# Performance work log

Measured on AMD Instinct MI355X. Metric: run time of the kernel, lower is better.

Reference implementation:

```python
import jax, jax.numpy as jnp
import numpy as np

D_MODEL = 1024
NHEAD = 16
HEAD_DIM = D_MODEL // NHEAD
WINDOW = 64


def setup_inputs() -> dict:
    key = jax.random.key(0)
    ks = jax.random.split(key, 5)
    B, S = 1, 4096
    x = jax.random.normal(ks[0], (B, S, D_MODEL), dtype=jnp.float32)
    scale = 0.02
    Wq = jax.random.normal(ks[1], (D_MODEL, D_MODEL), dtype=jnp.float32) * scale
    Wk = jax.random.normal(ks[2], (D_MODEL, D_MODEL), dtype=jnp.float32) * scale
    Wv = jax.random.normal(ks[3], (D_MODEL, D_MODEL), dtype=jnp.float32) * scale
    Wo = jax.random.normal(ks[4], (D_MODEL, D_MODEL), dtype=jnp.float32) * scale
    return {"x": x, "Wq": Wq, "Wk": Wk, "Wv": Wv, "Wo": Wo}


def reference(x, Wq, Wk, Wv, Wo):
    B, S, D = x.shape
    H, hd, W = NHEAD, HEAD_DIM, WINDOW
    # projections (torch Linear: y = x @ W.T)
    q = (x @ Wq.T).reshape(B, S, H, hd).transpose(0, 2, 1, 3)  # [B,H,S,hd]
    k = (x @ Wk.T).reshape(B, S, H, hd).transpose(0, 2, 1, 3)
    v = (x @ Wv.T).reshape(B, S, H, hd).transpose(0, 2, 1, 3)
    # sliding window indices: each query attends to [i-W+1, i]
    qpos = jnp.arange(S)
    offsets = jnp.arange(-W + 1, 1)
    key_idx = qpos[:, None] + offsets[None, :]          # [S,W]
    valid = (key_idx >= 0) & (key_idx < S)
    key_idx = jnp.clip(key_idx, 0, S - 1)
    # gather windows: [B,H,S,W,hd]
    kw = jnp.take(k, key_idx, axis=2)
    vw = jnp.take(v, key_idx, axis=2)
    scores = jnp.einsum('bhsd,bhswd->bhsw', q, kw) / (hd ** 0.5)
    scores = jnp.where(valid[None, None, :, :], scores, -jnp.inf)
    attn = jax.nn.softmax(scores, axis=-1)
    out = jnp.einsum('bhsw,bhswd->bhsd', attn, vw)      # [B,H,S,hd]
    out = out.transpose(0, 2, 1, 3).reshape(B, S, D)
    return out @ Wo.T
```

## Files before the change

### kernel.cpp

```cpp
#include <hip/hip_runtime.h>
#include <cstdint>

typedef unsigned short u16;
using bf16x8 = __attribute__((ext_vector_type(8))) short;
using u16x8  = __attribute__((ext_vector_type(8))) unsigned short;
using f32x4  = __attribute__((ext_vector_type(4))) float;

#define DM 1024

__device__ __forceinline__ u16 f2b(float f) {
    union { float f; unsigned u; } v; v.f = f;
    unsigned r = v.u + 0x7FFFu + ((v.u >> 16) & 1u);
    return (u16)(r >> 16);
}

#define GLL(gp, lp) __builtin_amdgcn_global_load_lds( \
    (const __attribute__((address_space(1))) void*)(uintptr_t)(gp), \
    (__attribute__((address_space(3))) void*)(unsigned)(uintptr_t)(lp), 16, 0, 0)

#define BAR()    __builtin_amdgcn_s_barrier()
#define WAITV6() asm volatile("s_waitcnt vmcnt(6)" ::: "memory")
#define WAITV5() asm volatile("s_waitcnt vmcnt(5)" ::: "memory")
#define WAITV0() asm volatile("s_waitcnt vmcnt(0)" ::: "memory")

__global__ __launch_bounds__(256) void cvt_all(const float* __restrict__ x,
                                               const float* __restrict__ Wq,
                                               const float* __restrict__ Wk,
                                               const float* __restrict__ Wv,
                                               const float* __restrict__ Wo,
                                               u16* __restrict__ xb,
                                               u16* __restrict__ wqkv,
                                               u16* __restrict__ wob) {
    size_t v = ((size_t)blockIdx.x * 256 + threadIdx.x) << 3;
    const float* src; u16* dst; size_t off; float sc = 1.0f;
    if (v < (size_t)4194304) { src = x; dst = xb; off = v; }
    else {
        size_t w = v - 4194304; int s = (int)(w >> 20); off = w & 1048575;
        src = (s == 0) ? Wq : (s == 1) ? Wk : (s == 2) ? Wv : Wo;
        dst = (s < 3) ? (wqkv + ((size_t)s << 20)) : wob;
        if (s == 0) sc = 0.125f;
    }
    const f32x4* p = (const f32x4*)(src + off);
    f32x4 a = p[0], b = p[1];
    u16x8 o;
    o[0] = f2b(a[0] * sc); o[1] = f2b(a[1] * sc); o[2] = f2b(a[2] * sc); o[3] = f2b(a[3] * sc);
    o[4] = f2b(b[0] * sc); o[5] = f2b(b[1] * sc); o[6] = f2b(b[2] * sc); o[7] = f2b(b[3] * sc);
    *(u16x8*)(dst + off) = o;
}

#define MROW3(af_, bf_, d) \
    acc[d][0] = __builtin_amdgcn_mfma_f32_16x16x32_bf16(af_, bf_[0], acc[d][0], 0, 0, 0); \
    acc[d][1] = __builtin_amdgcn_mfma_f32_16x16x32_bf16(af_, bf_[1], acc[d][1], 0, 0, 0); \
    acc[d][2] = __builtin_amdgcn_mfma_f32_16x16x32_bf16(af_, bf_[2], acc[d][2], 0, 0, 0);

#define MFMA12(af_, bf_) do { \
    __builtin_amdgcn_s_setprio(1); \
    MROW3(af_[0], bf_, 0) \
    MROW3(af_[1], bf_, 1) \
    MROW3(af_[2], bf_, 2) \
    MROW3(af_[3], bf_, 3) \
    __builtin_amdgcn_s_setprio(0); } while (0)

__global__ __launch_bounds__(512, 4) void gemm_qkv8(const u16* __restrict__ A,
                                                    const u16* __restrict__ B,
                                                    u16* __restrict__ QKV) {
    __shared__ __align__(16) u16 As[2 * 8192];
    __shared__ __align__(16) u16 Bs[2 * 12288];
    const int tid  = threadIdx.x;
    const int lane = tid & 63;
    const int wid  = tid >> 6;
    const int wr   = wid >> 2;
    const int wc   = wid & 3;
    const int fr   = lane & 15;
    const int fg   = lane >> 4;

    const int hw  = blockIdx.y * 16 + blockIdx.x;
    const int xcd = hw & 7;
    const int idx = hw >> 3;
    const int reg = xcd + ((idx >> 4) << 3);
    const int mt  = ((reg >> 2) << 2) + ((idx & 15) >> 2);
    const int nt  = ((reg & 3) << 2) + (idx & 3);
    const int brow = mt << 7;
    const int bcol = nt * 192;

    const int srow = tid >> 3;
    const int scol = ((tid & 7) ^ (srow & 7)) << 3;
    const u16* Ag = A + (size_t)(brow + srow) * 1024 + scol;
    const u16* Bg = B + (size_t)(bcol + srow) * 1024 + scol;

#define STG_A(buf, kt, c) GLL(Ag + (size_t)(c) * 65536 + (kt) * 64, \
                              (char*)As + (buf) * 16384 + (c) * 8192 + (wid << 10))
#define STG_B(buf, kt, c) GLL(Bg + (size_t)(c) * 65536 + (kt) * 64, \
                              (char*)Bs + (buf) * 24576 + (c) * 8192 + (wid << 10))
#define STG(buf, kt) do { \
        STG_A(buf, kt, 0); STG_A(buf, kt, 1); \
        STG_B(buf, kt, 0); STG_B(buf, kt, 1); STG_B(buf, kt, 2); } while (0)

    const int swz  = (fr & 7) << 3;
    const int col0 = (fg << 3) ^ swz;
    const int col1 = (32 + (fg << 3)) ^ swz;
    const int aro  = ((wr << 6) + fr) << 6;
    const int bro  = ((wc * 48) + fr) << 6;

#define LDA4(dst, bufo, cl) do { \
    const u16* p_ = As + (bufo) + aro + (cl); \
    dst[0] = *(const bf16x8*)(p_); \
    dst[1] = *(const bf16x8*)(p_ + 1024); \
    dst[2] = *(const bf16x8*)(p_ + 2048); \
    dst[3] = *(const bf16x8*)(p_ + 3072); } while (0)

#define LDB3(dst, bufo, cl) do { \
    const u16* p_ = Bs + (bufo) + bro + (cl); \
    dst[0] = *(const bf16x8*)(p_); \
    dst[1] = *(const bf16x8*)(p_ + 1024); \
    dst[2] = *(const bf16x8*)(p_ + 2048); } while (0)

    f32x4 acc[4][3];
    const f32x4 z = {0.f, 0.f, 0.f, 0.f};
    #pragma unroll
    for (int i = 0; i < 4; ++i)
        #pragma unroll
        for (int j = 0; j < 3; ++j) acc[i][j] = z;

    bf16x8 af0[4], af1[4], bf0[3], bf1[3];

    STG(0, 0);
    STG(1, 1);

    #pragma unroll 1
    for (int t = 0; t < 14; ++t) {
        const int bo  = (t & 1) ? 8192 : 0;
        const int bob = (t & 1) ? 12288 : 0;
        WAITV5();
        BAR();
        LDA4(af0, bo, col0); LDB3(bf0, bob, col0);
        MFMA12(af0, bf0);
        LDA4(af1, bo, col1); LDB3(bf1, bob, col1);
        MFMA12(af1, bf1);
        BAR();
        STG(t & 1, t + 2);
    }
    WAITV5(); BAR();
    LDA4(af0, 0, col0); LDB3(bf0, 0, col0);
    MFMA12(af0, bf0);
    LDA4(af1, 0, col1); LDB3(bf1, 0, col1);
    MFMA12(af1, bf1);
    WAITV0(); BAR();
    LDA4(af0, 8192, col0); LDB3(bf0, 12288, col0);
    MFMA12(af0, bf0);
    LDA4(af1, 8192, col1); LDB3(bf1, 12288, col1);
    MFMA12(af1, bf1);

    const int ocol0 = bcol + wc * 48;
    const int orow0 = brow + (wr << 6);
    #pragma unroll
    for (int i = 0; i < 4; ++i)
        #pragma unroll
        for (int j = 0; j < 3; ++j)
            #pragma unroll
            for (int r = 0; r < 4; ++r) {
                const int row = orow0 + i * 16 + fg * 4 + r;
                const int col = ocol0 + j * 16 + fr;
                QKV[(size_t)row * 3072 + col] = f2b(acc[i][j][r]);
            }
#undef STG_A
#undef STG_B
#undef STG
#undef LDA4
#undef LDB3
}

__global__ __launch_bounds__(256) void gemm_out(const u16* __restrict__ A,
                                                const u16* __restrict__ B,
                                                float* __restrict__ C) {
    __shared__ __align__(16) u16 As[2 * 8192];
    __shared__ __align__(16) u16 Bs[2 * 4096];
    const int tid  = threadIdx.x;
    const int lane = tid & 63;
    const int wid  = tid >> 6;
    const int wr   = wid >> 1;
    const int wc   = wid & 1;
    const int fr   = lane & 15;
    const int fg   = lane >> 4;

    const int hw  = blockIdx.y * 16 + blockIdx.x;
    const int xcd = hw & 7;
    const int idx = hw >> 3;
    const int reg = xcd + ((idx >> 4) << 3);
    const int mt  = ((reg >> 2) << 2) + ((idx & 15) >> 2);
    const int nt  = ((reg & 3) << 2) + (idx & 3);
    const int brow = mt << 7;
    const int bcol = nt << 6;

    const int srow = tid >> 3;
    const int scol = ((tid & 7) ^ (srow & 7)) << 3;
    const u16* Ag = A + (size_t)(brow + srow) * 1024 + scol;
    const u16* Bg = B + (size_t)(bcol + srow) * 1024 + scol;

#define OSTG_A(buf, kt, c) GLL(Ag + (size_t)(c) * 32768 + (kt) * 64, \
                               (char*)As + (buf) * 16384 + (c) * 4096 + (tid << 4))
#define OSTG_B(buf, kt, c) GLL(Bg + (size_t)(c) * 32768 + (kt) * 64, \
                               (char*)Bs + (buf) * 8192 + (c) * 4096 + (tid << 4))
#define OSTG(buf, kt) do { \
        OSTG_A(buf, kt, 0); OSTG_A(buf, kt, 1); OSTG_A(buf, kt, 2); OSTG_A(buf, kt, 3); \
        OSTG_B(buf, kt, 0); OSTG_B(buf, kt, 1); } while (0)

    const int swz  = (fr & 7) << 3;
    const int col0 = (fg << 3) ^ swz;
    const int col1 = (32 + (fg << 3)) ^ swz;
    const int aro  = ((wr << 6) + fr) << 6;
    const int bro  = ((wc << 5) + fr) << 6;

    f32x4 acc[4][2];
    const f32x4 z = {0.f, 0.f, 0.f, 0.f};
    #pragma unroll
    for (int i = 0; i < 4; ++i) { acc[i][0] = z; acc[i][1] = z; }

#define OCOMP(bufo4, bufo3) do { \
        const u16* Ab = As + (bufo4); \
        const u16* Bb = Bs + (bufo3); \
        bf16x8 a0[4], a1[4], b0[2], b1[2]; \
        _Pragma("unroll") \
        for (int i = 0; i < 4; ++i) { \
            a0[i] = *(const bf16x8*)(Ab + aro + (i << 10) + col0); \
            a1[i] = *(const bf16x8*)(Ab + aro + (i << 10) + col1); \
        } \
        _Pragma("unroll") \
        for (int j = 0; j < 2; ++j) { \
            b0[j] = *(const bf16x8*)(Bb + bro + (j << 10) + col0); \
            b1[j] = *(const bf16x8*)(Bb + bro + (j << 10) + col1); \
        } \
        __builtin_amdgcn_s_setprio(1); \
        _Pragma("unroll") \
        for (int i = 0; i < 4; ++i) \
            _Pragma("unroll") \
            for (int j = 0; j < 2; ++j) { \
                acc[i][j] = __builtin_amdgcn_mfma_f32_16x16x32_bf16(a0[i], b0[j], acc[i][j], 0, 0, 0); \
                acc[i][j] = __builtin_amdgcn_mfma_f32_16x16x32_bf16(a1[i], b1[j], acc[i][j], 0, 0, 0); \
            } \
        __builtin_amdgcn_s_setprio(0); } while (0)

    OSTG(0, 0);
    OSTG(1, 1);

    #pragma unroll 1
    for (int t = 0; t < 14; ++t) {
        const int bo4 = (t & 1) ? 8192 : 0;
        const int bo3 = (t & 1) ? 4096 : 0;
        WAITV6();
        BAR();
        OCOMP(bo4, bo3);
        BAR();
        OSTG(t & 1, t + 2);
    }
    WAITV6(); BAR();
    OCOMP(0, 0);
    WAITV0(); BAR();
    OCOMP(8192, 4096);
#undef OSTG_A
#undef OSTG_B
#undef OSTG
#undef OCOMP

    #pragma unroll
    for (int i = 0; i < 4; ++i)
        #pragma unroll
        for (int j = 0; j < 2; ++j)
            #pragma unroll
            for (int r = 0; r < 4; ++r) {
                const int row = brow + wr * 64 + i * 16 + fg * 4 + r;
                const int col = bcol + wc * 32 + j * 16 + fr;
                C[(size_t)row * 1024 + col] = acc[i][j][r];
            }
}

__global__ __launch_bounds__(256) void attn_kernel(const u16* __restrict__ QKV,
                                                   u16* __restrict__ Og) {
    const int qb  = blockIdx.x;
    const int h   = blockIdx.y;
    const int tid = threadIdx.x;
    const int lane = tid & 63;
    const int w  = tid >> 6;
    const int fr = lane & 15;
    const int fg = lane >> 4;

    __shared__ __align__(16) u16 QK[64 * 72 + 128 * 72];
    __shared__ __align__(16) u16 Vt[64 * 138];
    __shared__ float Mrow[64][4];
    __shared__ float Lrow[64][4];

    u16* Qs = QK;
    u16* Ks = QK + 64 * 72;
    u16* Ps = QK;

    const u16* Qg = QKV;
    const u16* Kg = QKV + 1024;
    const u16* Vg = QKV + 2048;

    const int hoff  = h * 64;
    const int qrow0 = qb * 64;
    const int krow0 = qrow0 - 64;

    {
        const int r  = tid >> 3;
        const int c0 = (tid & 7) * 8;
        #pragma unroll
        for (int it = 0; it < 2; ++it) {
            const int row = r + it * 32;
            u16x8 val = *(const u16x8*)(Qg + (size_t)(qrow0 + row) * 3072 + hoff + c0);
            *(u16x8*)(Qs + row * 72 + c0) = val;
        }
        #pragma unroll
        for (int it = 0; it < 4; ++it) {
            const int row  = r + it * 32;
            const int grow = krow0 + row;
            u16x8 val = {0, 0, 0, 0, 0, 0, 0, 0};
            if (grow >= 0) val = *(const u16x8*)(Kg + (size_t)grow * 3072 + hoff + c0);
            *(u16x8*)(Ks + row * 72 + c0) = val;
        }
        #pragma unroll
        for (int it = 0; it < 4; ++it) {
            const int j    = r + it * 32;
            const int grow = krow0 + j;
            u16x8 val = {0, 0, 0, 0, 0, 0, 0, 0};
            if (grow >= 0) val = *(const u16x8*)(Vg + (size_t)grow * 3072 + hoff + c0);
            #pragma unroll
            for (int e = 0; e < 8; ++e) Vt[(c0 + e) * 138 + j] = val[e];
        }
    }
    __syncthreads();

    const f32x4 z = {0.f, 0.f, 0.f, 0.f};
    f32x4 s[4][2];
    #pragma unroll
    for (int i = 0; i < 4; ++i) { s[i][0] = z; s[i][1] = z; }
    #pragma unroll
    for (int kk = 0; kk < 2; ++kk) {
        const int k0 = kk * 32 + fg * 8;
        bf16x8 aq[4];
        #pragma unroll
        for (int i = 0; i < 4; ++i)
            aq[i] = *(const bf16x8*)(Qs + (i * 16 + fr) * 72 + k0);
        #pragma unroll
        for (int n = 0; n < 2; ++n) {
            const bf16x8 bk = *(const bf16x8*)(Ks + (w * 32 + n * 16 + fr) * 72 + k0);
            #pragma unroll
            for (int i = 0; i < 4; ++i)
                s[i][n] = __builtin_amdgcn_mfma_f32_16x16x32_bf16(aq[i], bk, s[i][n], 0, 0, 0);
        }
    }

    #pragma unroll
    for (int i = 0; i < 4; ++i) {
        #pragma unroll
        for (int r = 0; r < 4; ++r) {
            const int irow = i * 16 + fg * 4 + r;
            float mx = -3.0e38f;
            #pragma unroll
            for (int n = 0; n < 2; ++n) {
                const int jcol = w * 32 + n * 16 + fr;
                const bool valid = (jcol >= irow + 1) && (jcol <= irow + 64) && (krow0 + jcol >= 0);
                const float v = valid ? s[i][n][r] : -3.0e38f;
                s[i][n][r] = v;
                mx = fmaxf(mx, v);
            }
            #pragma unroll
            for (int d = 1; d < 16; d <<= 1) mx = fmaxf(mx, __shfl_xor(mx, d));
            if (fr == 0) Mrow[irow][w] = mx;
        }
    }
    __syncthreads();

    #pragma unroll
    for (int i = 0; i < 4; ++i) {
        #pragma unroll
        for (int r = 0; r < 4; ++r) {
            const int irow = i * 16 + fg * 4 + r;
            const float M = fmaxf(fmaxf(Mrow[irow][0], Mrow[irow][1]),
                                  fmaxf(Mrow[irow][2], Mrow[irow][3]));
            float sum = 0.f;
            #pragma unroll
            for (int n = 0; n < 2; ++n) {
                const float v = s[i][n][r];
                const float p = (v > -1.0e38f) ? __expf(v - M) : 0.f;
                sum += p;
                Ps[irow * 136 + (w * 32 + n * 16 + fr)] = f2b(p);
            }
            #pragma unroll
            for (int d = 1; d < 16; d <<= 1) sum += __shfl_xor(sum, d);
            if (fr == 0) Lrow[irow][w] = sum;
        }
    }
    __syncthreads();

    f32x4 o[4] = {z, z, z, z};
    #pragma unroll
    for (int ks = 0; ks < 4; ++ks) {
        const int k0 = ks * 32 + fg * 8;
        const bf16x8 ap = *(const bf16x8*)(Ps + (w * 16 + fr) * 136 + k0);
        #pragma unroll
        for (int n = 0; n < 4; ++n) {
            const bf16x8 bv = *(const bf16x8*)(Vt + (n * 16 + fr) * 138 + k0);
            o[n] = __builtin_amdgcn_mfma_f32_16x16x32_bf16(ap, bv, o[n], 0, 0, 0);
        }
    }

    #pragma unroll
    for (int r = 0; r < 4; ++r) {
        const int irow = w * 16 + fg * 4 + r;
        const float L = Lrow[irow][0] + Lrow[irow][1] + Lrow[irow][2] + Lrow[irow][3];
        const float rl = 1.0f / L;
        #pragma unroll
        for (int n = 0; n < 4; ++n)
            Og[(size_t)(qrow0 + irow) * DM + hoff + n * 16 + fr] = f2b(o[n][r] * rl);
    }
}

extern "C" void kernel_launch(void* const* d_in, const int* in_sizes, int n_in,
                              void* d_out, int out_size, void* d_ws, size_t ws_size,
                              hipStream_t stream) {
    (void)in_sizes; (void)n_in; (void)out_size; (void)ws_size;
    const float* x  = (const float*)d_in[0];
    const float* Wq = (const float*)d_in[1];
    const float* Wk = (const float*)d_in[2];
    const float* Wv = (const float*)d_in[3];
    const float* Wo = (const float*)d_in[4];
    float* out = (float*)d_out;

    char* ws = (char*)d_ws;
    u16* xb   = (u16*)(ws);
    u16* Wqkv = (u16*)(ws + ((size_t)8  << 20));
    u16* Wob  = (u16*)(ws + ((size_t)14 << 20));
    u16* qkvb = (u16*)(ws + ((size_t)16 << 20));
    u16* ab   = (u16*)(ws + ((size_t)40 << 20));

    cvt_all<<<4096, 256, 0, stream>>>(x, Wq, Wk, Wv, Wo, xb, Wqkv, Wob);
    gemm_qkv8<<<dim3(16, 32), 512, 0, stream>>>(xb, Wqkv, qkvb);
    attn_kernel<<<dim3(64, 16), 256, 0, stream>>>(qkvb, ab);
    gemm_out<<<dim3(16, 32), 256, 0, stream>>>(ab, Wob, out);
}
```

Baseline: 79.75 us.

## Fuse fp32-to-bf16 conversion into GEMM staging and drop separate convert kernel

Removes the standalone conversion kernel and has both GEMMs load fp32 x/weights directly, convert to bf16 in registers (applying the Q scale), and write swizzled tiles into LDS via register prefetch. The aim is to save a kernel launch and the extra write/read of bf16 copies in global memory. The trade-off is that GEMM staging moves from async global-to-LDS loads to register-based loads with conversion ALU work. It also reads twice as many bytes per tile, and the QKV GEMM's occupancy hint drops from 4 to 2 waves per SIMD. x is re-read and re-converted by each of the 16 column tiles.

```diff
diff --git a/kernel.cpp b/kernel.cpp
--- a/kernel.cpp
+++ b/kernel.cpp
@@ -14,39 +14,21 @@
     return (u16)(r >> 16);
 }
 
+__device__ __forceinline__ u16x8 cvt8(f32x4 a, f32x4 b, float sc) {
+    u16x8 o;
+    o[0] = f2b(a[0] * sc); o[1] = f2b(a[1] * sc);
+    o[2] = f2b(a[2] * sc); o[3] = f2b(a[3] * sc);
+    o[4] = f2b(b[0] * sc); o[5] = f2b(b[1] * sc);
+    o[6] = f2b(b[2] * sc); o[7] = f2b(b[3] * sc);
+    return o;
+}
+
 #define GLL(gp, lp) __builtin_amdgcn_global_load_lds( \
     (const __attribute__((address_space(1))) void*)(uintptr_t)(gp), \
     (__attribute__((address_space(3))) void*)(unsigned)(uintptr_t)(lp), 16, 0, 0)
 
 #define BAR()    __builtin_amdgcn_s_barrier()
-#define WAITV6() asm volatile("s_waitcnt vmcnt(6)" ::: "memory")
-#define WAITV5() asm volatile("s_waitcnt vmcnt(5)" ::: "memory")
 #define WAITV0() asm volatile("s_waitcnt vmcnt(0)" ::: "memory")
-
-__global__ __launch_bounds__(256) void cvt_all(const float* __restrict__ x,
-                                               const float* __restrict__ Wq,
-                                               const float* __restrict__ Wk,
-                                               const float* __restrict__ Wv,
-                                               const float* __restrict__ Wo,
-                                               u16* __restrict__ xb,
-                                               u16* __restrict__ wqkv,
-                                               u16* __restrict__ wob) {
-    size_t v = ((size_t)blockIdx.x * 256 + threadIdx.x) << 3;
-    const float* src; u16* dst; size_t off; float sc = 1.0f;
-    if (v < (size_t)4194304) { src = x; dst = xb; off = v; }
-    else {
-        size_t w = v - 4194304; int s = (int)(w >> 20); off = w & 1048575;
-        src = (s == 0) ? Wq : (s == 1) ? Wk : (s == 2) ? Wv : Wo;
-        dst = (s < 3) ? (wqkv + ((size_t)s << 20)) : wob;
-        if (s == 0) sc = 0.125f;
-    }
-    const f32x4* p = (const f32x4*)(src + off);
-    f32x4 a = p[0], b = p[1];
-    u16x8 o;
-    o[0] = f2b(a[0] * sc); o[1] = f2b(a[1] * sc); o[2] = f2b(a[2] * sc); o[3] = f2b(a[3] * sc);
-    o[4] = f2b(b[0] * sc); o[5] = f2b(b[1] * sc); o[6] = f2b(b[2] * sc); o[7] = f2b(b[3] * sc);
-    *(u16x8*)(dst + off) = o;
-}
 
 #define MROW3(af_, bf_, d) \
     acc[d][0] = __builtin_amdgcn_mfma_f32_16x16x32_bf16(af_, bf_[0], acc[d][0], 0, 0, 0); \
@@ -61,8 +43,10 @@
     MROW3(af_[3], bf_, 3) \
     __builtin_amdgcn_s_setprio(0); } while (0)
 
-__global__ __launch_bounds__(512, 4) void gemm_qkv8(const u16* __restrict__ A,
-                                                    const u16* __restrict__ B,
+__global__ __launch_bounds__(512, 2) void gemm_qkv8(const float* __restrict__ x,
+                                                    const float* __restrict__ Wq,
+                                                    const float* __restrict__ Wk,
+                                                    const float* __restrict__ Wv,
                                                     u16* __restrict__ QKV) {
     __shared__ __align__(16) u16 As[2 * 8192];
     __shared__ __align__(16) u16 Bs[2 * 12288];
@@ -84,17 +68,49 @@
     const int bcol = nt * 192;
 
     const int srow = tid >> 3;
-    const int scol = ((tid & 7) ^ (srow & 7)) << 3;
-    const u16* Ag = A + (size_t)(brow + srow) * 1024 + scol;
-    const u16* Bg = B + (size_t)(bcol + srow) * 1024 + scol;
-
-#define STG_A(buf, kt, c) GLL(Ag + (size_t)(c) * 65536 + (kt) * 64, \
-                              (char*)As + (buf) * 16384 + (c) * 8192 + (wid << 10))
-#define STG_B(buf, kt, c) GLL(Bg + (size_t)(c) * 65536 + (kt) * 64, \
-                              (char*)Bs + (buf) * 24576 + (c) * 8192 + (wid << 10))
-#define STG(buf, kt) do { \
-        STG_A(buf, kt, 0); STG_A(buf, kt, 1); \
-        STG_B(buf, kt, 0); STG_B(buf, kt, 1); STG_B(buf, kt, 2); } while (0)
+    const int cg   = tid & 7;
+    const int aD   = srow * 64 + ((cg ^ (srow & 7)) << 3);
+
+    const float* aSrc0 = x + (size_t)(brow + srow) * 1024 + cg * 8;
+    const float* aSrc1 = x + (size_t)(brow + 64 + srow) * 1024 + cg * 8;
+    const float* bSrc0; const float* bSrc1; const float* bSrc2;
+    float bScl0, bScl1, bScl2;
+    {
+        int g0 = bcol + srow, g1 = bcol + 64 + srow, g2 = bcol + 128 + srow;
+        bSrc0 = ((g0 < 1024) ? (Wq + (size_t)g0 * 1024)
+                 : (g0 < 2048) ? (Wk + (size_t)(g0 - 1024) * 1024)
+                               : (Wv + (size_t)(g0 - 2048) * 1024)) + cg * 8;
+        bScl0 = (g0 < 1024) ? 0.125f : 1.0f;
+        bSrc1 = ((g1 < 1024) ? (Wq + (size_t)g1 * 1024)
+                 : (g1 < 2048) ? (Wk + (size_t)(g1 - 1024) * 1024)
+                               : (Wv + (size_t)(g1 - 2048) * 1024)) + cg * 8;
+        bScl1 = (g1 < 1024) ? 0.125f : 1.0f;
+        bSrc2 = ((g2 < 1024) ? (Wq + (size_t)g2 * 1024)
+                 : (g2 < 2048) ? (Wk + (size_t)(g2 - 1024) * 1024)
+                               : (Wv + (size_t)(g2 - 2048) * 1024)) + cg * 8;
+        bScl2 = (g2 < 1024) ? 0.125f : 1.0f;
+    }
+
+    f32x4 la00, la01, la10, la11;
+    f32x4 lb00, lb01, lb10, lb11, lb20, lb21;
+
+#define ISSUE(kt) do { \
+    la00 = *(const f32x4*)(aSrc0 + (kt) * 64); la01 = *(const f32x4*)(aSrc0 + (kt) * 64 + 4); \
+    la10 = *(const f32x4*)(aSrc1 + (kt) * 64); la11 = *(const f32x4*)(aSrc1 + (kt) * 64 + 4); \
+    lb00 = *(const f32x4*)(bSrc0 + (kt) * 64); lb01 = *(const f32x4*)(bSrc0 + (kt) * 64 + 4); \
+    lb10 = *(const f32x4*)(bSrc1 + (kt) * 64); lb11 = *(const f32x4*)(bSrc1 + (kt) * 64 + 4); \
+    lb20 = *(const f32x4*)(bSrc2 + (kt) * 64); lb21 = *(const f32x4*)(bSrc2 + (kt) * 64 + 4); \
+} while (0)
+
+#define WRITE(bi) do { \
+    u16* Ad = As + (bi) * 8192 + aD; \
+    u16* Bd = Bs + (bi) * 12288 + aD; \
+    *(u16x8*)(Ad)        = cvt8(la00, la01, 1.0f); \
+    *(u16x8*)(Ad + 4096) = cvt8(la10, la11, 1.0f); \
+    *(u16x8*)(Bd)        = cvt8(lb00, lb01, bScl0); \
+    *(u16x8*)(Bd + 4096) = cvt8(lb10, lb11, bScl1); \
+    *(u16x8*)(Bd + 8192) = cvt8(lb20, lb21, bScl2); \
+} while (0)
 
     const int swz  = (fr & 7) << 3;
     const int col0 = (fg << 3) ^ swz;
@@ -124,28 +140,24 @@
 
     bf16x8 af0[4], af1[4], bf0[3], bf1[3];
 
-    STG(0, 0);
-    STG(1, 1);
+    ISSUE(0);
+    WRITE(0);
+    ISSUE(1);
 
     #pragma unroll 1
-    for (int t = 0; t < 14; ++t) {
+    for (int t = 0; t < 15; ++t) {
         const int bo  = (t & 1) ? 8192 : 0;
         const int bob = (t & 1) ? 12288 : 0;
-        WAITV5();
         BAR();
         LDA4(af0, bo, col0); LDB3(bf0, bob, col0);
         MFMA12(af0, bf0);
         LDA4(af1, bo, col1); LDB3(bf1, bob, col1);
         MFMA12(af1, bf1);
         BAR();
-        STG(t & 1, t + 2);
-    }
-    WAITV5(); BAR();
-    LDA4(af0, 0, col0); LDB3(bf0, 0, col0);
-    MFMA12(af0, bf0);
-    LDA4(af1, 0, col1); LDB3(bf1, 0, col1);
-    MFMA12(af1, bf1);
-    WAITV0(); BAR();
+        WRITE((t + 1) & 1);
+        if (t < 14) ISSUE(t + 2);
+    }
+    BAR();
     LDA4(af0, 8192, col0); LDB3(bf0, 12288, col0);
     MFMA12(af0, bf0);
     LDA4(af1, 8192, col1); LDB3(bf1, 12288, col1);
@@ -163,15 +175,14 @@
                 const int col = ocol0 + j * 16 + fr;
                 QKV[(size_t)row * 3072 + col] = f2b(acc[i][j][r]);
             }
-#undef STG_A
-#undef STG_B
-#undef STG
+#undef ISSUE
+#undef WRITE
 #undef LDA4
 #undef LDB3
 }
 
 __global__ __launch_bounds__(256) void gemm_out(const u16* __restrict__ A,
-                                                const u16* __restrict__ B,
+                                                const float* __restrict__ Wo,
                                                 float* __restrict__ C) {
     __shared__ __align__(16) u16 As[2 * 8192];
     __shared__ __align__(16) u16 Bs[2 * 4096];
@@ -193,17 +204,24 @@
     const int bcol = nt << 6;
 
     const int srow = tid >> 3;
-    const int scol = ((tid & 7) ^ (srow & 7)) << 3;
+    const int cg   = tid & 7;
+    const int scol = ((cg ^ (srow & 7)) << 3);
     const u16* Ag = A + (size_t)(brow + srow) * 1024 + scol;
-    const u16* Bg = B + (size_t)(bcol + srow) * 1024 + scol;
+    const float* bSrc0 = Wo + (size_t)(bcol + srow) * 1024 + cg * 8;
+    const float* bSrc1 = Wo + (size_t)(bcol + 32 + srow) * 1024 + cg * 8;
+    const int bD = srow * 64 + ((cg ^ (srow & 7)) << 3);
 
 #define OSTG_A(buf, kt, c) GLL(Ag + (size_t)(c) * 32768 + (kt) * 64, \
                                (char*)As + (buf) * 16384 + (c) * 4096 + (tid << 4))
-#define OSTG_B(buf, kt, c) GLL(Bg + (size_t)(c) * 32768 + (kt) * 64, \
-                               (char*)Bs + (buf) * 8192 + (c) * 4096 + (tid << 4))
-#define OSTG(buf, kt) do { \
-        OSTG_A(buf, kt, 0); OSTG_A(buf, kt, 1); OSTG_A(buf, kt, 2); OSTG_A(buf, kt, 3); \
-        OSTG_B(buf, kt, 0); OSTG_B(buf, kt, 1); } while (0)
+#define OSTGA(buf, kt) do { \
+        OSTG_A(buf, kt, 0); OSTG_A(buf, kt, 1); OSTG_A(buf, kt, 2); OSTG_A(buf, kt, 3); } while (0)
+#define OISSUE(kt) do { \
+    lb00 = *(const f32x4*)(bSrc0 + (kt) * 64); lb01 = *(const f32x4*)(bSrc0 + (kt) * 64 + 4); \
+    lb10 = *(const f32x4*)(bSrc1 + (kt) * 64); lb11 = *(const f32x4*)(bSrc1 + (kt) * 64 + 4); } while (0)
+#define OWRITE(bi) do { \
+    u16* Bd = Bs + (bi) * 4096 + bD; \
+    *(u16x8*)(Bd)        = cvt8(lb00, lb01, 1.0f); \
+    *(u16x8*)(Bd + 2048) = cvt8(lb10, lb11, 1.0f); } while (0)
 
     const int swz  = (fr & 7) << 3;
     const int col0 = (fg << 3) ^ swz;
@@ -215,6 +233,7 @@
     const f32x4 z = {0.f, 0.f, 0.f, 0.f};
     #pragma unroll
     for (int i = 0; i < 4; ++i) { acc[i][0] = z; acc[i][1] = z; }
+    f32x4 lb00, lb01, lb10, lb11;
 
 #define OCOMP(bufo4, bufo3) do { \
         const u16* Ab = As + (bufo4); \
@@ -240,26 +259,28 @@
             } \
         __builtin_amdgcn_s_setprio(0); } while (0)
 
-    OSTG(0, 0);
-    OSTG(1, 1);
+    OSTGA(0, 0); OISSUE(0);
+    WAITV0();
+    OWRITE(0);
+    OSTGA(1, 1); OISSUE(1);
 
     #pragma unroll 1
-    for (int t = 0; t < 14; ++t) {
+    for (int t = 0; t < 15; ++t) {
         const int bo4 = (t & 1) ? 8192 : 0;
         const int bo3 = (t & 1) ? 4096 : 0;
-        WAITV6();
         BAR();
         OCOMP(bo4, bo3);
         BAR();
-        OSTG(t & 1, t + 2);
-    }
-    WAITV6(); BAR();
-    OCOMP(0, 0);
-    WAITV0(); BAR();
+        WAITV0();
+        OWRITE((t + 1) & 1);
+        if (t < 14) { OSTGA(t & 1, t + 2); OISSUE(t + 2); }
+    }
+    BAR();
     OCOMP(8192, 4096);
 #undef OSTG_A
-#undef OSTG_B
-#undef OSTG
+#undef OSTGA
+#undef OISSUE
+#undef OWRITE
 #undef OCOMP
 
     #pragma unroll
@@ -428,14 +449,10 @@
     float* out = (float*)d_out;
 
     char* ws = (char*)d_ws;
-    u16* xb   = (u16*)(ws);
-    u16* Wqkv = (u16*)(ws + ((size_t)8  << 20));
-    u16* Wob  = (u16*)(ws + ((size_t)14 << 20));
-    u16* qkvb = (u16*)(ws + ((size_t)16 << 20));
-    u16* ab   = (u16*)(ws + ((size_t)40 << 20));
-
-    cvt_all<<<4096, 256, 0, stream>>>(x, Wq, Wk, Wv, Wo, xb, Wqkv, Wob);
-    gemm_qkv8<<<dim3(16, 32), 512, 0, stream>>>(xb, Wqkv, qkvb);
+    u16* qkvb = (u16*)(ws);
+    u16* ab   = (u16*)(ws + ((size_t)24 << 20));
+
+    gemm_qkv8<<<dim3(16, 32), 512, 0, stream>>>(x, Wq, Wk, Wv, qkvb);
     attn_kernel<<<dim3(64, 16), 256, 0, stream>>>(qkvb, ab);
-    gemm_out<<<dim3(16, 32), 256, 0, stream>>>(ab, Wob, out);
-}
+    gemm_out<<<dim3(16, 32), 256, 0, stream>>>(ab, Wo, out);
+}
```

Measured after the change: 100.2 us. 25.7% more time.
